# Performance work log

Hardware: AMD Instinct MI355X
Metric: run time of the kernel (lower is better)

Reference implementation:

```python
import jax, jax.numpy as jnp
import numpy as np

SIZE = 7
SIGMA = 1.5
K1 = 0.01
K2 = 0.03
DATA_RANGE = 2.0
NP_ = SIZE * SIZE
COV_NORM = NP_ / (NP_ - 1)
PAD = SIZE // 2


def _gaussian_window(size=SIZE, sigma=SIGMA, channels=1):
    x = np.arange(size) - size // 2
    g = np.exp(-x**2 / (2.0 * sigma**2))[None, :]
    g = (g.T @ g)
    g = g / g.sum()
    w = np.tile(g[None, None], (channels, 1, 1, 1))  # [C,1,size,size]
    return jnp.asarray(w, dtype=jnp.float32)


def _dwconv(x, w):
    # depthwise conv2d, zero padding PAD, stride 1; x: [N,C,H,W], w: [C,1,k,k]
    c = x.shape[1]
    return jax.lax.conv_general_dilated(
        x, w, window_strides=(1, 1), padding=[(PAD, PAD), (PAD, PAD)],
        dimension_numbers=('NCHW', 'OIHW', 'NCHW'), feature_group_count=c)


def setup_inputs() -> dict:
    key = jax.random.key(0)
    k1, k2 = jax.random.split(key)
    X = jax.random.uniform(k1, (64, 1, 320, 320), dtype=jnp.float32)
    Y = jax.random.uniform(k2, (64, 1, 320, 320), dtype=jnp.float32)
    window = _gaussian_window()
    return {"X": X, "Y": Y, "window": window}


def reference(X, Y, window):
    C1 = (K1 * DATA_RANGE) ** 2
    C2 = (K2 * DATA_RANGE) ** 2
    mux = _dwconv(X, window)
    muy = _dwconv(Y, window)
    mux_sq = mux * mux
    muy_sq = muy * muy
    muxy = mux * muy
    sigmax_sq = (_dwconv(X * X, window) - mux_sq) * COV_NORM
    sigmay_sq = (_dwconv(Y * Y, window) - muy_sq) * COV_NORM
    sigmaxy = (_dwconv(X * Y, window) - muxy) * COV_NORM
    ssim_map = ((2 * muxy + C1) * (2 * sigmaxy + C2)) / \
               ((mux_sq + muy_sq + C1) * (sigmax_sq + sigmay_sq + C2))
    return 1.0 - ssim_map.mean()
```

## Files before the change

kernel.cpp:

```cpp
#include <hip/hip_runtime.h>
#include <math.h>


#define WI 320
#define HI 320
#define NI 64
#define TWO 58
#define GXD 6
#define GYD 20
#define NBLK (GXD * GYD * NI)
#define NPIX ((double)NI * WI * HI)
#define WREG (5 * 4 * 64)

typedef float v4 __attribute__((ext_vector_type(4)));

struct W7 { float w[7]; };

template <bool YI, int XM>
__device__ __forceinline__ float wave_task(
    const float* __restrict__ Xn, const float* __restrict__ Yn,
    const W7& wv, float* __restrict__ vb, int x0, int y0, int lane)
{
    const int gx   = x0 + lane - 3;
    const bool xok = (XM == 1) || (XM == 0 ? (gx >= 0) : (gx < WI));

    float xr[10], yr[10];
#pragma unroll
    for (int j = 0; j < 10; ++j) {
        const int gy  = y0 + j - 3;
        const bool ok = xok && (YI || ((unsigned)gy < (unsigned)HI));
        float xv = 0.f, yv = 0.f;
        if (ok) { const int idx = gy * WI + gx; xv = Xn[idx]; yv = Yn[idx]; }
        xr[j] = xv; yr[j] = yv;
    }

    float acc[5][4];
#pragma unroll
    for (int ch = 0; ch < 5; ++ch)
#pragma unroll
        for (int r = 0; r < 4; ++r) acc[ch][r] = 0.f;
#pragma unroll
    for (int j = 0; j < 10; ++j) {
        const float xv = xr[j], yv = yr[j];
        const float pxx = xv * xv, pyy = yv * yv, pxy = xv * yv;
#pragma unroll
        for (int r = 0; r < 4; ++r) {
            const int d = j - r;
            if (d >= 0 && d < 7) {
                const float w = wv.w[d];
                acc[0][r] += w * xv;
                acc[1][r] += w * yv;
                acc[2][r] += w * pxx;
                acc[3][r] += w * pyy;
                acc[4][r] += w * pxy;
            }
        }
    }
#pragma unroll
    for (int ch = 0; ch < 5; ++ch)
#pragma unroll
        for (int r = 0; r < 4; ++r)
            vb[ch * 256 + r * 64 + lane] = acc[ch][r];

    __builtin_amdgcn_wave_barrier();

    float lsum = 0.f;
    const int row = lane >> 4;
    const int xg  = (lane & 15) << 2;
    if (xg < TWO) {
        const float C1 = 0.0004f, C2 = 0.0036f, COVN = 49.f / 48.f;
        float m[4][5];
#pragma unroll
        for (int j = 0; j < 4; ++j)
#pragma unroll
            for (int ch = 0; ch < 5; ++ch) m[j][ch] = 0.f;
#pragma unroll
        for (int ch = 0; ch < 5; ++ch) {
            const v4* p = (const v4*)&vb[ch * 256 + row * 64 + xg];
            v4 a = p[0], b = p[1], c = p[2];
            float f[12] = {a.x,a.y,a.z,a.w, b.x,b.y,b.z,b.w, c.x,c.y,c.z,c.w};
#pragma unroll
            for (int j = 0; j < 4; ++j) {
                float s = 0.f;
#pragma unroll
                for (int d = 0; d < 7; ++d) s += wv.w[d] * f[j + d];
                m[j][ch] = s;
            }
        }
#pragma unroll
        for (int j = 0; j < 4; ++j) {
            const float mx = m[j][0], my = m[j][1];
            const float mxsq = mx * mx;
            const float mysq = my * my;
            const float mxy  = mx * my;
            const float vx   = (m[j][2] - mxsq) * COVN;
            const float vy   = (m[j][3] - mysq) * COVN;
            const float vxy  = (m[j][4] - mxy)  * COVN;
            const float num  = (2.f * mxy + C1) * (2.f * vxy + C2);
            const float den  = (mxsq + mysq + C1) * (vx + vy + C2);
            const bool valid = (xg + j < TWO) && (XM != 2 || x0 + xg + j < WI);
            lsum += valid ? num * __builtin_amdgcn_rcpf(den) : 0.f;
        }
    }
    return lsum;
}

__global__ __launch_bounds__(256) void ssim_kernel(
    const float* __restrict__ X, const float* __restrict__ Y,
    W7 wv, float* __restrict__ partial)
{
    __shared__ __align__(16) float vbuf[4 * WREG + 16];
    __shared__ float wsum[4];

    const int tid  = threadIdx.x;
    const int lane = tid & 63;
    const int w    = tid >> 6;
    const int x0   = blockIdx.x * TWO;
    const int y0   = blockIdx.y * 16 + w * 4;
    const float* __restrict__ Xn = X + (size_t)blockIdx.z * (WI * HI);
    const float* __restrict__ Yn = Y + (size_t)blockIdx.z * (WI * HI);
    float* vb = vbuf + w * WREG;

    const bool yi = (y0 >= 3) && (y0 <= HI - 7);
    const int  xm = (blockIdx.x == 0) ? 0 : ((blockIdx.x == GXD - 1) ? 2 : 1);

    float lsum;
    if (yi) {
        if      (xm == 0) lsum = wave_task<true, 0>(Xn, Yn, wv, vb, x0, y0, lane);
        else if (xm == 1) lsum = wave_task<true, 1>(Xn, Yn, wv, vb, x0, y0, lane);
        else              lsum = wave_task<true, 2>(Xn, Yn, wv, vb, x0, y0, lane);
    } else {
        if      (xm == 0) lsum = wave_task<false, 0>(Xn, Yn, wv, vb, x0, y0, lane);
        else if (xm == 1) lsum = wave_task<false, 1>(Xn, Yn, wv, vb, x0, y0, lane);
        else              lsum = wave_task<false, 2>(Xn, Yn, wv, vb, x0, y0, lane);
    }

#pragma unroll
    for (int off = 32; off > 0; off >>= 1)
        lsum += __shfl_down(lsum, off, 64);
    if (lane == 0) wsum[w] = lsum;
    __syncthreads();
    if (tid == 0) {
        const int bid = (blockIdx.z * GYD + blockIdx.y) * GXD + blockIdx.x;
        partial[bid] = (wsum[0] + wsum[1]) + (wsum[2] + wsum[3]);
    }
}

__global__ __launch_bounds__(256) void ssim_finalize(
    const float* __restrict__ partial, float* __restrict__ out)
{
    __shared__ double ws[4];
    const int tid = threadIdx.x;
    double s = 0.0;
    for (int i = tid; i < NBLK; i += 256) s += (double)partial[i];
#pragma unroll
    for (int off = 32; off > 0; off >>= 1)
        s += __shfl_down(s, off, 64);
    if ((tid & 63) == 0) ws[tid >> 6] = s;
    __syncthreads();
    if (tid == 0)
        out[0] = (float)(1.0 - ((ws[0] + ws[1]) + (ws[2] + ws[3])) / NPIX);
}

extern "C" void kernel_launch(void* const* d_in, const int* in_sizes, int n_in,
                              void* d_out, int out_size, void* d_ws, size_t ws_size,
                              hipStream_t stream) {
    const float* X = (const float*)d_in[0];
    const float* Y = (const float*)d_in[1];
    W7 wv;
    {
        double g[7], s = 0.0;
        for (int i = 0; i < 7; ++i) {
            double x = (double)(i - 3);
            g[i] = exp(-(x * x) / (2.0 * 1.5 * 1.5));
            s += g[i];
        }
        for (int i = 0; i < 7; ++i) wv.w[i] = (float)(g[i] / s);
    }

    float* partial = (float*)d_ws;

    dim3 grid(GXD, GYD, NI);
    ssim_kernel<<<grid, 256, 0, stream>>>(X, Y, wv, partial);
    ssim_finalize<<<1, 256, 0, stream>>>(partial, (float*)d_out);
}
```

Before: 110.8 us.

## Use single-wave blocks looping over row strips with double-buffered register prefetch

Each block is now one 64-thread wavefront that walks eight 4-row strips, covering 32 rows. It prefetches the next strip's X/Y column into a second register set while computing the current one. The aim is to hide global load latency inside each wave and cut per-block overhead such as the cross-wave LDS reduction and __syncthreads. In exchange the grid holds far fewer waves, which reduces occupancy-based latency hiding. The templated bounds-check specialisations are also dropped, so every load now carries runtime bounds checks.

Result: no change. 112.7 us (+1.7%).

```diff
diff --git a/kernel.cpp b/kernel.cpp
--- a/kernel.cpp
+++ b/kernel.cpp
@@ -7,33 +7,34 @@
 #define NI 64
 #define TWO 58
 #define GXD 6
-#define GYD 20
+#define RPB 32
+#define ITERS 8
+#define GYD 10
 #define NBLK (GXD * GYD * NI)
 #define NPIX ((double)NI * WI * HI)
-#define WREG (5 * 4 * 64)
 
 typedef float v4 __attribute__((ext_vector_type(4)));
 
 struct W7 { float w[7]; };
 
-template <bool YI, int XM>
-__device__ __forceinline__ float wave_task(
+__device__ __forceinline__ void issue_loads(
     const float* __restrict__ Xn, const float* __restrict__ Yn,
-    const W7& wv, float* __restrict__ vb, int x0, int y0, int lane)
+    int gx, bool xok, int ybase, float (&xr)[10], float (&yr)[10])
 {
-    const int gx   = x0 + lane - 3;
-    const bool xok = (XM == 1) || (XM == 0 ? (gx >= 0) : (gx < WI));
-
-    float xr[10], yr[10];
 #pragma unroll
     for (int j = 0; j < 10; ++j) {
-        const int gy  = y0 + j - 3;
-        const bool ok = xok && (YI || ((unsigned)gy < (unsigned)HI));
+        const int gy  = ybase + j;
+        const bool ok = xok && ((unsigned)gy < (unsigned)HI);
         float xv = 0.f, yv = 0.f;
         if (ok) { const int idx = gy * WI + gx; xv = Xn[idx]; yv = Yn[idx]; }
         xr[j] = xv; yr[j] = yv;
     }
+}
 
+__device__ __forceinline__ float compute_strip(
+    const W7& wv, float* __restrict__ vb,
+    const float (&xr)[10], const float (&yr)[10], int lane, int maxc)
+{
     float acc[5][4];
 #pragma unroll
     for (int ch = 0; ch < 5; ++ch)
@@ -64,85 +65,80 @@
 
     __builtin_amdgcn_wave_barrier();
 
-    float lsum = 0.f;
     const int row = lane >> 4;
     const int xg  = (lane & 15) << 2;
-    if (xg < TWO) {
-        const float C1 = 0.0004f, C2 = 0.0036f, COVN = 49.f / 48.f;
-        float m[4][5];
+    const float C1 = 0.0004f, C2 = 0.0036f, COVN = 49.f / 48.f;
+
+    float m[4][5];
 #pragma unroll
-        for (int j = 0; j < 4; ++j)
+    for (int j = 0; j < 4; ++j)
 #pragma unroll
-            for (int ch = 0; ch < 5; ++ch) m[j][ch] = 0.f;
+        for (int ch = 0; ch < 5; ++ch) m[j][ch] = 0.f;
 #pragma unroll
-        for (int ch = 0; ch < 5; ++ch) {
-            const v4* p = (const v4*)&vb[ch * 256 + row * 64 + xg];
-            v4 a = p[0], b = p[1], c = p[2];
-            float f[12] = {a.x,a.y,a.z,a.w, b.x,b.y,b.z,b.w, c.x,c.y,c.z,c.w};
-#pragma unroll
-            for (int j = 0; j < 4; ++j) {
-                float s = 0.f;
-#pragma unroll
-                for (int d = 0; d < 7; ++d) s += wv.w[d] * f[j + d];
-                m[j][ch] = s;
-            }
-        }
+    for (int ch = 0; ch < 5; ++ch) {
+        const v4* p = (const v4*)&vb[ch * 256 + row * 64 + xg];
+        v4 a = p[0], b = p[1], c = p[2];
+        float f[12] = {a.x,a.y,a.z,a.w, b.x,b.y,b.z,b.w, c.x,c.y,c.z,c.w};
 #pragma unroll
         for (int j = 0; j < 4; ++j) {
-            const float mx = m[j][0], my = m[j][1];
-            const float mxsq = mx * mx;
-            const float mysq = my * my;
-            const float mxy  = mx * my;
-            const float vx   = (m[j][2] - mxsq) * COVN;
-            const float vy   = (m[j][3] - mysq) * COVN;
-            const float vxy  = (m[j][4] - mxy)  * COVN;
-            const float num  = (2.f * mxy + C1) * (2.f * vxy + C2);
-            const float den  = (mxsq + mysq + C1) * (vx + vy + C2);
-            const bool valid = (xg + j < TWO) && (XM != 2 || x0 + xg + j < WI);
-            lsum += valid ? num * __builtin_amdgcn_rcpf(den) : 0.f;
+            float s = 0.f;
+#pragma unroll
+            for (int d = 0; d < 7; ++d) s += wv.w[d] * f[j + d];
+            m[j][ch] = s;
         }
+    }
+    float lsum = 0.f;
+#pragma unroll
+    for (int j = 0; j < 4; ++j) {
+        const float mx = m[j][0], my = m[j][1];
+        const float mxsq = mx * mx;
+        const float mysq = my * my;
+        const float mxy  = mx * my;
+        const float vx   = (m[j][2] - mxsq) * COVN;
+        const float vy   = (m[j][3] - mysq) * COVN;
+        const float vxy  = (m[j][4] - mxy)  * COVN;
+        const float num  = (2.f * mxy + C1) * (2.f * vxy + C2);
+        const float den  = (mxsq + mysq + C1) * (vx + vy + C2);
+        lsum += (xg + j < maxc) ? num * __builtin_amdgcn_rcpf(den) : 0.f;
     }
     return lsum;
 }
 
-__global__ __launch_bounds__(256) void ssim_kernel(
+__global__ __launch_bounds__(64) void ssim_kernel(
     const float* __restrict__ X, const float* __restrict__ Y,
     W7 wv, float* __restrict__ partial)
 {
-    __shared__ __align__(16) float vbuf[4 * WREG + 16];
-    __shared__ float wsum[4];
+    __shared__ __align__(16) float vbuf[5 * 4 * 64 + 16];
 
-    const int tid  = threadIdx.x;
-    const int lane = tid & 63;
-    const int w    = tid >> 6;
+    const int lane = threadIdx.x;
     const int x0   = blockIdx.x * TWO;
-    const int y0   = blockIdx.y * 16 + w * 4;
+    const int y0   = blockIdx.y * RPB;
     const float* __restrict__ Xn = X + (size_t)blockIdx.z * (WI * HI);
     const float* __restrict__ Yn = Y + (size_t)blockIdx.z * (WI * HI);
-    float* vb = vbuf + w * WREG;
 
-    const bool yi = (y0 >= 3) && (y0 <= HI - 7);
-    const int  xm = (blockIdx.x == 0) ? 0 : ((blockIdx.x == GXD - 1) ? 2 : 1);
+    const int  gx   = x0 + lane - 3;
+    const bool xok  = (unsigned)gx < (unsigned)WI;
+    const int  maxc = (x0 + TWO <= WI) ? TWO : (WI - x0);
 
-    float lsum;
-    if (yi) {
-        if      (xm == 0) lsum = wave_task<true, 0>(Xn, Yn, wv, vb, x0, y0, lane);
-        else if (xm == 1) lsum = wave_task<true, 1>(Xn, Yn, wv, vb, x0, y0, lane);
-        else              lsum = wave_task<true, 2>(Xn, Yn, wv, vb, x0, y0, lane);
-    } else {
-        if      (xm == 0) lsum = wave_task<false, 0>(Xn, Yn, wv, vb, x0, y0, lane);
-        else if (xm == 1) lsum = wave_task<false, 1>(Xn, Yn, wv, vb, x0, y0, lane);
-        else              lsum = wave_task<false, 2>(Xn, Yn, wv, vb, x0, y0, lane);
+    float ax[10], ay[10], bx[10], by[10];
+    issue_loads(Xn, Yn, gx, xok, y0 - 3, ax, ay);
+
+    float lsum = 0.f;
+#pragma unroll 1
+    for (int ii = 0; ii < ITERS; ii += 2) {
+        issue_loads(Xn, Yn, gx, xok, y0 + 4 * (ii + 1) - 3, bx, by);
+        lsum += compute_strip(wv, vbuf, ax, ay, lane, maxc);
+        if (ii + 2 < ITERS)
+            issue_loads(Xn, Yn, gx, xok, y0 + 4 * (ii + 2) - 3, ax, ay);
+        lsum += compute_strip(wv, vbuf, bx, by, lane, maxc);
     }
 
 #pragma unroll
     for (int off = 32; off > 0; off >>= 1)
         lsum += __shfl_down(lsum, off, 64);
-    if (lane == 0) wsum[w] = lsum;
-    __syncthreads();
-    if (tid == 0) {
+    if (lane == 0) {
         const int bid = (blockIdx.z * GYD + blockIdx.y) * GXD + blockIdx.x;
-        partial[bid] = (wsum[0] + wsum[1]) + (wsum[2] + wsum[3]);
+        partial[bid] = lsum;
     }
 }
 
@@ -181,6 +177,6 @@
     float* partial = (float*)d_ws;
 
     dim3 grid(GXD, GYD, NI);
-    ssim_kernel<<<grid, 256, 0, stream>>>(X, Y, wv, partial);
+    ssim_kernel<<<grid, 64, 0, stream>>>(X, Y, wv, partial);
     ssim_finalize<<<1, 256, 0, stream>>>(partial, (float*)d_out);
 }
```
